# Kernel optimization log

Measured on AMD Instinct MI355X. Metric: run time of the kernel, lower is better.

The kernel has to match this reference:

```python
import jax, jax.numpy as jnp
import numpy as np

B = 4096      # batch (must equal hidden for the denom broadcast, see notes)
D = 2048      # input_size
P = 4096      # input_size * proj_factor
H = 4096      # hidden_size
NH = 16       # num_heads
HS = H // NH  # head_size = 256
EPS = 1e-5


def setup_inputs() -> dict:
    key = jax.random.key(0)
    ks = jax.random.split(key, 20)
    r = lambda i, shape, s=1.0: jax.random.normal(ks[i], shape, dtype=jnp.float32) * s
    w = 0.02
    return dict(
        x=r(0, (B, D)), h_prev=r(1, (B, H)), c_prev=r(2, (B, H)),
        n_prev=r(3, (B, H)), m_prev=r(4, (B, H)),
        ln_g=jnp.ones((D,), jnp.float32), ln_b=jnp.zeros((D,), jnp.float32),
        W_upL=r(5, (D, P), w), b_upL=jnp.zeros((P,), jnp.float32),
        W_upR=r(6, (D, H), w), b_upR=jnp.zeros((H,), jnp.float32),
        conv_w=r(7, (1, 1, 4), 0.5), conv_b=jnp.zeros((1,), jnp.float32),
        W_skip=r(8, (P, H), w), b_skip=jnp.zeros((H,), jnp.float32),
        Wq_w=r(9, (NH, P // NH, HS), w), Wq_b=jnp.zeros((H,), jnp.float32),
        Wk_w=r(10, (NH, P // NH, HS), w), Wk_b=jnp.zeros((H,), jnp.float32),
        Wv_w=r(11, (NH, P // NH, HS), w), Wv_b=jnp.zeros((H,), jnp.float32),
        Wi_w=r(12, (P, H), w), Wi_b=jnp.zeros((H,), jnp.float32),
        Wf_w=r(13, (P, H), w), Wf_b=jnp.zeros((H,), jnp.float32),
        Wo_w=r(14, (P, H), w), Wo_b=jnp.zeros((H,), jnp.float32),
        gn_g=jnp.ones((H,), jnp.float32), gn_b=jnp.zeros((H,), jnp.float32),
        W_down=r(15, (H, D), w), b_down=jnp.zeros((D,), jnp.float32),
    )


def _block_diag(x, w, b):
    # x: [B, nh*block_in], w: [nh, block_in, block_out] -> [B, nh*block_out]
    nh = w.shape[0]
    xr = x.reshape(x.shape[0], nh, -1)
    return jnp.einsum('bni,nio->bno', xr, w).reshape(x.shape[0], -1) + b


def reference(x, h_prev, c_prev, n_prev, m_prev, ln_g, ln_b,
              W_upL, b_upL, W_upR, b_upR, conv_w, conv_b, W_skip, b_skip,
              Wq_w, Wq_b, Wk_w, Wk_b, Wv_w, Wv_b,
              Wi_w, Wi_b, Wf_w, Wf_b, Wo_w, Wo_b,
              gn_g, gn_b, W_down, b_down):
    # LayerNorm over input_size
    mu = x.mean(-1, keepdims=True)
    var = x.var(-1, keepdims=True)
    x_norm = (x - mu) / jnp.sqrt(var + EPS) * ln_g + ln_b

    x_left = x_norm @ W_upL + b_upL    # [B, P]
    x_right = x_norm @ W_upR + b_upR   # [B, H]

    # CausalConv1D(1,1,4): left-pad 3 == pad both sides by 3 then trim right 3
    xc = jax.lax.conv_general_dilated(
        x_left[:, None, :], conv_w, (1,), [(3, 0)],
        dimension_numbers=('NCH', 'OIH', 'NCH')) + conv_b[None, :, None]
    x_conv = jax.nn.silu(xc[:, 0, :])  # [B, P]

    x_skip = x_conv @ W_skip + b_skip  # [B, H]

    q = _block_diag(x_conv, Wq_w, Wq_b)
    k = _block_diag(x_conv, Wk_w, Wk_b) / jnp.sqrt(jnp.float32(HS))
    v = _block_diag(x_left, Wv_w, Wv_b)

    i_tilde = x_conv @ Wi_w + Wi_b
    f_tilde = x_conv @ Wf_w + Wf_b
    o = jax.nn.sigmoid(x_left @ Wo_w + Wo_b)

    # stabilized exponential gating
    m_t = jnp.maximum(f_tilde + m_prev, i_tilde)
    i_g = jnp.exp(i_tilde - m_t)
    f_g = jnp.exp(f_tilde + m_prev - m_t)

    c_t = f_g * c_prev + i_g * (v * k)
    n_t = f_g * n_prev + i_g * k

    denom = jnp.maximum(jnp.abs(n_t.T @ q), 1.0)  # [H, H]; B == H so elementwise below
    h_t = o * (c_t * q) / denom                    # [B, H]

    # GroupNorm(num_heads, hidden) on 2D input [B, H]
    hg = h_t.reshape(B, NH, HS)
    gmu = hg.mean(-1, keepdims=True)
    gvar = hg.var(-1, keepdims=True)
    gn = ((hg - gmu) / jnp.sqrt(gvar + EPS)).reshape(B, H) * gn_g + gn_b

    out = (gn + x_skip) * jax.nn.silu(x_right)
    out = out @ W_down + b_down
    return (out + x, h_t, c_t, n_t, m_t)
```

## Files before the change

kernel.cpp:

```cpp
#include <hip/hip_runtime.h>
#include <math.h>

constexpr int BB = 4096;
constexpr int DD = 2048;
constexpr int PP = 4096;
constexpr int HH = 4096;
constexpr int NH = 16;
constexpr int HS = 256;

using bf16 = __bf16;
typedef __attribute__((ext_vector_type(8))) __bf16 bf16x8;
typedef __attribute__((ext_vector_type(2))) __bf16 bf16x2;
typedef __attribute__((ext_vector_type(4))) float  floatx4;

__device__ __forceinline__ void gl_lds16(const bf16* g, bf16* l) {
    __builtin_amdgcn_global_load_lds(
        (__attribute__((address_space(1))) void*)g,
        (__attribute__((address_space(3))) void*)l,
        16, 0, 0);
}

__global__ void ln_kernel(const float* __restrict__ x, const float* __restrict__ g,
                          const float* __restrict__ b, bf16* __restrict__ xn) {
    int row = blockIdx.x;
    int tid = threadIdx.x;
    const float* xr = x + (long)row * DD;
    float v[8];
    float s1 = 0.f, s2 = 0.f;
#pragma unroll
    for (int i = 0; i < 8; ++i) {
        v[i] = xr[tid + 256 * i];
        s1 += v[i]; s2 += v[i] * v[i];
    }
    for (int off = 32; off > 0; off >>= 1) {
        s1 += __shfl_down(s1, off);
        s2 += __shfl_down(s2, off);
    }
    __shared__ float r1[4], r2[4];
    if ((tid & 63) == 0) { r1[tid >> 6] = s1; r2[tid >> 6] = s2; }
    __syncthreads();
    float t1 = r1[0] + r1[1] + r1[2] + r1[3];
    float t2 = r2[0] + r2[1] + r2[2] + r2[3];
    float mu  = t1 * (1.f / DD);
    float var = t2 * (1.f / DD) - mu * mu;
    float inv = rsqrtf(var + 1e-5f);
    bf16* xo = xn + (long)row * DD;
#pragma unroll
    for (int i = 0; i < 8; ++i) {
        int c = tid + 256 * i;
        xo[c] = (bf16)((v[i] - mu) * inv * g[c] + b[c]);
    }
}

__global__ __launch_bounds__(256)
void tconv_kernel(const float* __restrict__ in, bf16* __restrict__ out, int R, int C) {
    __shared__ float t[64][33];
    const long zo = (long)blockIdx.z * (long)R * C;
    in  += zo; out += zo;
    const int c0 = blockIdx.x * 32, r0 = blockIdx.y * 64;
    const int xx = threadIdx.x & 31, yy = threadIdx.x >> 5;
#pragma unroll
    for (int d = 0; d < 64; d += 8)
        t[yy + d][xx] = in[(long)(r0 + yy + d) * C + c0 + xx];
    __syncthreads();
#pragma unroll
    for (int d = 0; d < 32; d += 8) {
        const int cc = c0 + yy + d;
        bf16x2 pk;
        pk.x = (bf16)t[2 * xx + 0][yy + d];
        pk.y = (bf16)t[2 * xx + 1][yy + d];
        *reinterpret_cast<bf16x2*>(&out[(long)cc * R + r0 + 2 * xx]) = pk;
    }
}

__global__ void conv_silu_kernel(const float* __restrict__ xl, const float* __restrict__ w,
                                 const float* __restrict__ cb, bf16* __restrict__ xc) {
    long i = (long)blockIdx.x * 256 + threadIdx.x;
    int p = (int)(i & (PP - 1));
    const float* base = xl + (i - p);
    float acc = cb[0];
#pragma unroll
    for (int j = 0; j < 4; ++j) {
        int pp = p - 3 + j;
        if (pp >= 0) acc = fmaf(w[j], base[pp], acc);
    }
    xc[i] = (bf16)(acc / (1.f + expf(-acc)));
}

__global__ void gates_kernel(const float* __restrict__ it_, const float* __restrict__ ft_,
                             const float* __restrict__ mp, const float* __restrict__ cp,
                             const float* __restrict__ np, const float* __restrict__ kk,
                             const float* __restrict__ vv,
                             float* __restrict__ c_out, float* __restrict__ n_out,
                             float* __restrict__ m_out) {
    long i = (long)blockIdx.x * 256 + threadIdx.x;
    float it = it_[i], ft = ft_[i];
    float fm = ft + mp[i];
    float mt = fmaxf(fm, it);
    float ig = expf(it - mt);
    float fg = expf(fm - mt);
    float ks = kk[i] * 0.0625f;
    c_out[i] = fg * cp[i] + ig * (vv[i] * ks);
    n_out[i] = fg * np[i] + ig * ks;
    m_out[i] = mt;
}

__global__ void hgn_kernel(const float* __restrict__ o_pre, const float* __restrict__ ct,
                           const float* __restrict__ qm, const float* __restrict__ den,
                           const float* __restrict__ xs, const float* __restrict__ xr,
                           const float* __restrict__ gg, const float* __restrict__ gb,
                           float* __restrict__ h_out, bf16* __restrict__ s_out) {
    int blk = blockIdx.x;
    int b = blk >> 4, hd = blk & 15;
    int c = threadIdx.x;
    int gcol = hd * HS + c;
    long idx = (long)b * HH + gcol;
    float o  = 1.f / (1.f + expf(-o_pre[idx]));
    float ht = o * ct[idx] * qm[idx] / fmaxf(fabsf(den[idx]), 1.f);
    h_out[idx] = ht;
    float s1 = ht, s2 = ht * ht;
    for (int off = 32; off > 0; off >>= 1) {
        s1 += __shfl_down(s1, off);
        s2 += __shfl_down(s2, off);
    }
    __shared__ float r1[4], r2[4];
    if ((c & 63) == 0) { r1[c >> 6] = s1; r2[c >> 6] = s2; }
    __syncthreads();
    float t1 = r1[0] + r1[1] + r1[2] + r1[3];
    float t2 = r2[0] + r2[1] + r2[2] + r2[3];
    float mu  = t1 * (1.f / HS);
    float var = t2 * (1.f / HS) - mu * mu;
    float gn  = (ht - mu) * rsqrtf(var + 1e-5f) * gg[gcol] + gb[gcol];
    float xrv = xr[idx];
    float sil = xrv / (1.f + expf(-xrv));
    s_out[idx] = (bf16)((gn + xs[idx]) * sil);
}

template<bool WRITE_BF16, bool ADD_RES>
__global__ __launch_bounds__(256)
void gemm_nt(const bf16* __restrict__ A, int lda, long sAz,
             const bf16* __restrict__ Bt, int ldb, long sBz,
             const float* __restrict__ bias, int sbz,
             const float* __restrict__ res,
             float* __restrict__ C, int ldc, long sCz,
             bf16* __restrict__ Cb, int ldcb, long sCbz,
             int K) {
    __shared__ bf16 As[128 * 32];
    __shared__ bf16 Bs[128 * 32];
    const int tid = threadIdx.x;
    const int m0 = blockIdx.y * 128, n0 = blockIdx.x * 128, z = blockIdx.z;
    A  += (long)z * sAz;
    Bt += (long)z * sBz;
    C  += (long)z * sCz;
    if (bias) bias += (long)z * sbz;
    if (WRITE_BF16) Cb += (long)z * sCbz;

    const int lane = tid & 63, wave = tid >> 6;
    const int row = tid >> 2;
    const int kc  = (tid & 3) * 8;
    const bf16* ga = A  + (long)(m0 + row) * lda + kc;
    const bf16* gb = Bt + (long)(n0 + row) * ldb + kc;
    bf16* lA = As + wave * (16 * 32);
    bf16* lB = Bs + wave * (16 * 32);
    const long stepA = (long)64 * lda, stepB = (long)64 * ldb;

    const int wm = (wave >> 1) * 64, wn = (wave & 1) * 64;
    const int lr = lane & 15, qd = lane >> 4;
    floatx4 acc[4][4] = {};

    for (int k0 = 0; k0 < K; k0 += 32) {
        gl_lds16(ga,         lA);
        gl_lds16(ga + stepA, lA + 64 * 32);
        gl_lds16(gb,         lB);
        gl_lds16(gb + stepB, lB + 64 * 32);
        ga += 32; gb += 32;
        __syncthreads();

        bf16x8 af[4], bfv[4];
#pragma unroll
        for (int i = 0; i < 4; ++i)
            af[i]  = *reinterpret_cast<const bf16x8*>(&As[(wm + i * 16 + lr) * 32 + qd * 8]);
#pragma unroll
        for (int j = 0; j < 4; ++j)
            bfv[j] = *reinterpret_cast<const bf16x8*>(&Bs[(wn + j * 16 + lr) * 32 + qd * 8]);
#pragma unroll
        for (int i = 0; i < 4; ++i)
#pragma unroll
            for (int j = 0; j < 4; ++j)
                acc[i][j] = __builtin_amdgcn_mfma_f32_16x16x32_bf16(af[i], bfv[j], acc[i][j], 0, 0, 0);
        __syncthreads();
    }

#pragma unroll
    for (int i = 0; i < 4; ++i) {
        const int rowb = m0 + wm + i * 16 + qd * 4;
#pragma unroll
        for (int j = 0; j < 4; ++j) {
            const int col = n0 + wn + j * 16 + lr;
            const float bi = bias ? bias[col] : 0.f;
#pragma unroll
            for (int r = 0; r < 4; ++r) {
                const long gi = (long)(rowb + r) * ldc + col;
                float v0 = acc[i][j][r] + bi;
                if (ADD_RES) v0 += res[gi];
                C[gi] = v0;
                if (WRITE_BF16) Cb[(long)(rowb + r) * ldcb + col] = (bf16)v0;
            }
        }
    }
}

extern "C" void kernel_launch(void* const* d_in, const int* in_sizes, int n_in,
                              void* d_out, int out_size, void* d_ws, size_t ws_size,
                              hipStream_t stream) {
    const float* x      = (const float*)d_in[0];
    const float* c_prev = (const float*)d_in[2];
    const float* n_prev = (const float*)d_in[3];
    const float* m_prev = (const float*)d_in[4];
    const float* ln_g   = (const float*)d_in[5];
    const float* ln_b   = (const float*)d_in[6];
    const float* W_upL  = (const float*)d_in[7];
    const float* b_upL  = (const float*)d_in[8];
    const float* W_upR  = (const float*)d_in[9];
    const float* b_upR  = (const float*)d_in[10];
    const float* conv_w = (const float*)d_in[11];
    const float* conv_b = (const float*)d_in[12];
    const float* W_skip = (const float*)d_in[13];
    const float* b_skip = (const float*)d_in[14];
    const float* Wq_w   = (const float*)d_in[15];
    const float* Wq_b   = (const float*)d_in[16];
    const float* Wk_w   = (const float*)d_in[17];
    const float* Wk_b   = (const float*)d_in[18];
    const float* Wv_w   = (const float*)d_in[19];
    const float* Wv_b   = (const float*)d_in[20];
    const float* Wi_w   = (const float*)d_in[21];
    const float* Wi_b   = (const float*)d_in[22];
    const float* Wf_w   = (const float*)d_in[23];
    const float* Wf_b   = (const float*)d_in[24];
    const float* Wo_w   = (const float*)d_in[25];
    const float* Wo_b   = (const float*)d_in[26];
    const float* gn_g   = (const float*)d_in[27];
    const float* gn_b   = (const float*)d_in[28];
    const float* W_down = (const float*)d_in[29];
    const float* b_down = (const float*)d_in[30];

    float* out0  = (float*)d_out;
    float* h_out = out0  + (long)BB * DD;
    float* c_out = h_out + (long)BB * HH;
    float* n_out = c_out + (long)BB * HH;
    float* m_out = n_out + (long)BB * HH;

    float* ws = (float*)d_ws;
    const long SLOT = (long)BB * HH;
    float* s0 = ws + 0 * SLOT;
    float* s1 = ws + 1 * SLOT;
    float* s2 = ws + 2 * SLOT;
    float* s3 = ws + 3 * SLOT;
    float* s4 = ws + 4 * SLOT;
    float* s5 = ws + 5 * SLOT;
    float* s6 = ws + 6 * SLOT;
    float* s7 = ws + 7 * SLOT;
    float* s8 = ws + 8 * SLOT;

    float* xr   = s0;
    float* xs   = s1;
    float* it   = s2;
    float* den  = s2;
    float* ft   = s3;
    float* opre = s4;
    float* qbuf = s5;
    float* kbuf = s6;
    float* xl   = s7;
    float* vbuf = s7;

    bf16* xn_bf = (bf16*)s6;
    bf16* xl_bf = (bf16*)(s6 + SLOT / 4);
    bf16* nT_bf = (bf16*)s3;
    bf16* qT_bf = (bf16*)(s3 + SLOT / 2);
    bf16* wt    = (bf16*)s8;
    bf16* xc_bf = (bf16*)(s8 + SLOT / 2);
    bf16* s_bf  = (bf16*)s7;

    dim3 blk(256);

    ln_kernel<<<BB, blk, 0, stream>>>(x, ln_g, ln_b, xn_bf);

    tconv_kernel<<<dim3(PP / 32, DD / 64, 1), blk, 0, stream>>>(W_upL, wt, DD, PP);
    gemm_nt<true, false><<<dim3(PP / 128, BB / 128, 1), blk, 0, stream>>>(
        xn_bf, DD, 0, wt, DD, 0, b_upL, 0, nullptr, xl, PP, 0, xl_bf, PP, 0, DD);

    tconv_kernel<<<dim3(HH / 32, DD / 64, 1), blk, 0, stream>>>(W_upR, wt, DD, HH);
    gemm_nt<false, false><<<dim3(HH / 128, BB / 128, 1), blk, 0, stream>>>(
        xn_bf, DD, 0, wt, DD, 0, b_upR, 0, nullptr, xr, HH, 0, nullptr, 0, 0, DD);

    conv_silu_kernel<<<dim3((unsigned)((long)BB * PP / 256)), blk, 0, stream>>>(
        xl, conv_w, conv_b, xc_bf);

    tconv_kernel<<<dim3(HH / 32, PP / 64, 1), blk, 0, stream>>>(W_skip, wt, PP, HH);
    gemm_nt<false, false><<<dim3(HH / 128, BB / 128, 1), blk, 0, stream>>>(
        xc_bf, PP, 0, wt, PP, 0, b_skip, 0, nullptr, xs, HH, 0, nullptr, 0, 0, PP);

    tconv_kernel<<<dim3(HH / 32, PP / 64, 1), blk, 0, stream>>>(Wi_w, wt, PP, HH);
    gemm_nt<false, false><<<dim3(HH / 128, BB / 128, 1), blk, 0, stream>>>(
        xc_bf, PP, 0, wt, PP, 0, Wi_b, 0, nullptr, it, HH, 0, nullptr, 0, 0, PP);

    tconv_kernel<<<dim3(HH / 32, PP / 64, 1), blk, 0, stream>>>(Wf_w, wt, PP, HH);
    gemm_nt<false, false><<<dim3(HH / 128, BB / 128, 1), blk, 0, stream>>>(
        xc_bf, PP, 0, wt, PP, 0, Wf_b, 0, nullptr, ft, HH, 0, nullptr, 0, 0, PP);

    tconv_kernel<<<dim3(HH / 32, PP / 64, 1), blk, 0, stream>>>(Wo_w, wt, PP, HH);
    gemm_nt<false, false><<<dim3(HH / 128, BB / 128, 1), blk, 0, stream>>>(
        xl_bf, PP, 0, wt, PP, 0, Wo_b, 0, nullptr, opre, HH, 0, nullptr, 0, 0, PP);

    tconv_kernel<<<dim3(HS / 32, HS / 64, NH), blk, 0, stream>>>(Wq_w, wt, HS, HS);
    gemm_nt<false, false><<<dim3(HS / 128, BB / 128, NH), blk, 0, stream>>>(
        xc_bf, PP, HS, wt, HS, (long)HS * HS, Wq_b, HS, nullptr, qbuf, HH, HS,
        nullptr, 0, 0, HS);

    tconv_kernel<<<dim3(HS / 32, HS / 64, NH), blk, 0, stream>>>(Wv_w, wt, HS, HS);
    gemm_nt<false, false><<<dim3(HS / 128, BB / 128, NH), blk, 0, stream>>>(
        xl_bf, PP, HS, wt, HS, (long)HS * HS, Wv_b, HS, nullptr, vbuf, HH, HS,
        nullptr, 0, 0, HS);

    tconv_kernel<<<dim3(HS / 32, HS / 64, NH), blk, 0, stream>>>(Wk_w, wt, HS, HS);
    gemm_nt<false, false><<<dim3(HS / 128, BB / 128, NH), blk, 0, stream>>>(
        xc_bf, PP, HS, wt, HS, (long)HS * HS, Wk_b, HS, nullptr, kbuf, HH, HS,
        nullptr, 0, 0, HS);

    gates_kernel<<<dim3((unsigned)((long)BB * HH / 256)), blk, 0, stream>>>(
        it, ft, m_prev, c_prev, n_prev, kbuf, vbuf, c_out, n_out, m_out);

    tconv_kernel<<<dim3(HH / 32, BB / 64, 1), blk, 0, stream>>>(n_out, nT_bf, BB, HH);
    tconv_kernel<<<dim3(HH / 32, BB / 64, 1), blk, 0, stream>>>(qbuf, qT_bf, BB, HH);

    gemm_nt<false, false><<<dim3(HH / 128, HH / 128, 1), blk, 0, stream>>>(
        nT_bf, BB, 0, qT_bf, BB, 0, nullptr, 0, nullptr, den, HH, 0,
        nullptr, 0, 0, BB);

    hgn_kernel<<<dim3(BB * NH), blk, 0, stream>>>(
        opre, c_out, qbuf, den, xs, xr, gn_g, gn_b, h_out, s_bf);

    tconv_kernel<<<dim3(DD / 32, HH / 64, 1), blk, 0, stream>>>(W_down, wt, HH, DD);
    gemm_nt<false, true><<<dim3(DD / 128, BB / 128, 1), blk, 0, stream>>>(
        s_bf, HH, 0, wt, HH, 0, b_down, 0, x, out0, DD, 0, nullptr, 0, 0, HH);
}
```

Baseline: 2.517 ms.

## Replace GEMM with 256x256 double-buffered pipelined MFMA kernel with swizzled LDS

Replaces the 128x128 single-buffered GEMM with a 512-thread 256x256 tile kernel. It uses K=64 stages split in two halves, double-buffered LDS filled by async global-to-LDS loads, and an XOR swizzle on the LDS layout to avoid bank conflicts. Loads for the next stage are issued between MFMA groups under s_setprio, with explicit vmcnt waits and barriers in place of __syncthreads. The aim is to hide memory latency, raise arithmetic intensity per tile, and improve L2 reuse through block remapping on 16x16 grids. The costs are heavy LDS use (128KB), more register pressure, and fewer blocks for the small per-head GEMMs.

```diff
diff --git a/kernel.cpp b/kernel.cpp
--- a/kernel.cpp
+++ b/kernel.cpp
@@ -19,6 +19,9 @@
         (__attribute__((address_space(3))) void*)l,
         16, 0, 0);
 }
+
+#define WAITV(n) asm volatile("s_waitcnt vmcnt(" #n ")" ::: "memory")
+#define BAR()    asm volatile("s_barrier" ::: "memory")
 
 __global__ void ln_kernel(const float* __restrict__ x, const float* __restrict__ g,
                           const float* __restrict__ b, bf16* __restrict__ xn) {
@@ -137,66 +140,132 @@
 }
 
 template<bool WRITE_BF16, bool ADD_RES>
-__global__ __launch_bounds__(256)
-void gemm_nt(const bf16* __restrict__ A, int lda, long sAz,
+__global__ __launch_bounds__(512, 2)
+void gemm256(const bf16* __restrict__ A, int lda, long sAz,
              const bf16* __restrict__ Bt, int ldb, long sBz,
              const float* __restrict__ bias, int sbz,
              const float* __restrict__ res,
              float* __restrict__ C, int ldc, long sCz,
              bf16* __restrict__ Cb, int ldcb, long sCbz,
              int K) {
-    __shared__ bf16 As[128 * 32];
-    __shared__ bf16 Bs[128 * 32];
-    const int tid = threadIdx.x;
-    const int m0 = blockIdx.y * 128, n0 = blockIdx.x * 128, z = blockIdx.z;
+    __shared__ bf16 smA[2][2][8192];
+    __shared__ bf16 smB[2][2][8192];
+
+    const int tid  = threadIdx.x;
+    const int wave = tid >> 6, lane = tid & 63;
+
+    int bx = blockIdx.x, by = blockIdx.y;
+    if (gridDim.x == 16 && gridDim.y == 16) {
+        int bid = by * 16 + bx;
+        int r = bid & 7, i = bid >> 3;
+        by = (r >> 1) * 4 + (i >> 3);
+        bx = (r & 1) * 8 + (i & 7);
+    }
+    const int m0 = by * 256, n0 = bx * 256, z = blockIdx.z;
     A  += (long)z * sAz;
     Bt += (long)z * sBz;
     C  += (long)z * sCz;
     if (bias) bias += (long)z * sbz;
     if (WRITE_BF16) Cb += (long)z * sCbz;
 
-    const int lane = tid & 63, wave = tid >> 6;
-    const int row = tid >> 2;
-    const int kc  = (tid & 3) * 8;
-    const bf16* ga = A  + (long)(m0 + row) * lda + kc;
-    const bf16* gb = Bt + (long)(n0 + row) * ldb + kc;
-    bf16* lA = As + wave * (16 * 32);
-    bf16* lB = Bs + wave * (16 * 32);
-    const long stepA = (long)64 * lda, stepB = (long)64 * ldb;
-
-    const int wm = (wave >> 1) * 64, wn = (wave & 1) * 64;
+    const int srow = tid >> 2;
+    const int scol = ((tid & 3) ^ ((tid >> 3) & 3)) * 8;
+    const bf16* pA = A  + (long)(m0 + srow) * lda + scol;
+    const bf16* pB = Bt + (long)(n0 + srow) * ldb + scol;
+
+#define STAGE_A(dd, kkk, kcol) do { \
+    const bf16* _s = pA + (kcol) + (kkk) * 32; \
+    gl_lds16(_s,                   &smA[dd][kkk][wave * 512]); \
+    gl_lds16(_s + 128 * (long)lda, &smA[dd][kkk][4096 + wave * 512]); } while (0)
+#define STAGE_B(dd, kkk, kcol) do { \
+    const bf16* _s = pB + (kcol) + (kkk) * 32; \
+    gl_lds16(_s,                   &smB[dd][kkk][wave * 512]); \
+    gl_lds16(_s + 128 * (long)ldb, &smB[dd][kkk][4096 + wave * 512]); } while (0)
+#define LD8(base, off) (*reinterpret_cast<const bf16x8*>((const char*)(base) + (off)))
+
+    const int wr = wave >> 2, wc = wave & 3;
     const int lr = lane & 15, qd = lane >> 4;
-    floatx4 acc[4][4] = {};
-
-    for (int k0 = 0; k0 < K; k0 += 32) {
-        gl_lds16(ga,         lA);
-        gl_lds16(ga + stepA, lA + 64 * 32);
-        gl_lds16(gb,         lB);
-        gl_lds16(gb + stepB, lB + 64 * 32);
-        ga += 32; gb += 32;
-        __syncthreads();
-
-        bf16x8 af[4], bfv[4];
+    const int xorv = ((lr >> 1) & 3) << 4;
+    const int aoff = (wr * 128 + lr) * 64 + ((qd * 16) ^ xorv);
+    const int boff = (wc * 64  + lr) * 64 + ((qd * 16) ^ xorv);
+
+    floatx4 acc[8][4] = {};
+    const int nt = K >> 6;
+
+    STAGE_A(0, 0, 0); STAGE_B(0, 0, 0); STAGE_A(0, 1, 0); STAGE_B(0, 1, 0);
+    WAITV(4);
+    BAR();
+
+    for (int t = 0; t < nt; ++t) {
+        const int d = t & 1, e = d ^ 1;
+        const int kn = (t + 1 < nt) ? (t + 1) * 64 : 0;
+        const char* A0p = (const char*)&smA[d][0][0];
+        const char* A1p = (const char*)&smA[d][1][0];
+        const char* B0p = (const char*)&smB[d][0][0];
+        const char* B1p = (const char*)&smB[d][1][0];
+        bf16x8 af[4], bv[4];
+
+#pragma unroll
+        for (int i = 0; i < 4; ++i) af[i] = LD8(A0p, aoff + i * 1024);
+#pragma unroll
+        for (int j = 0; j < 4; ++j) bv[j] = LD8(B0p, boff + j * 1024);
+        STAGE_A(e, 0, kn);
+        __builtin_amdgcn_s_setprio(1);
 #pragma unroll
         for (int i = 0; i < 4; ++i)
-            af[i]  = *reinterpret_cast<const bf16x8*>(&As[(wm + i * 16 + lr) * 32 + qd * 8]);
-#pragma unroll
-        for (int j = 0; j < 4; ++j)
-            bfv[j] = *reinterpret_cast<const bf16x8*>(&Bs[(wn + j * 16 + lr) * 32 + qd * 8]);
+#pragma unroll
+            for (int j = 0; j < 4; ++j)
+                acc[i][j] = __builtin_amdgcn_mfma_f32_16x16x32_bf16(af[i], bv[j], acc[i][j], 0, 0, 0);
+        __builtin_amdgcn_s_setprio(0);
+        BAR();
+
+#pragma unroll
+        for (int i = 0; i < 4; ++i) af[i] = LD8(A0p, aoff + 4096 + i * 1024);
+        STAGE_B(e, 0, kn);
+        __builtin_amdgcn_s_setprio(1);
 #pragma unroll
         for (int i = 0; i < 4; ++i)
 #pragma unroll
             for (int j = 0; j < 4; ++j)
-                acc[i][j] = __builtin_amdgcn_mfma_f32_16x16x32_bf16(af[i], bfv[j], acc[i][j], 0, 0, 0);
-        __syncthreads();
-    }
-
-#pragma unroll
-    for (int i = 0; i < 4; ++i) {
-        const int rowb = m0 + wm + i * 16 + qd * 4;
+                acc[4 + i][j] = __builtin_amdgcn_mfma_f32_16x16x32_bf16(af[i], bv[j], acc[4 + i][j], 0, 0, 0);
+        __builtin_amdgcn_s_setprio(0);
+        WAITV(4);
+        BAR();
+
+#pragma unroll
+        for (int i = 0; i < 4; ++i) af[i] = LD8(A1p, aoff + i * 1024);
+#pragma unroll
+        for (int j = 0; j < 4; ++j) bv[j] = LD8(B1p, boff + j * 1024);
+        STAGE_A(e, 1, kn);
+        __builtin_amdgcn_s_setprio(1);
+#pragma unroll
+        for (int i = 0; i < 4; ++i)
+#pragma unroll
+            for (int j = 0; j < 4; ++j)
+                acc[i][j] = __builtin_amdgcn_mfma_f32_16x16x32_bf16(af[i], bv[j], acc[i][j], 0, 0, 0);
+        __builtin_amdgcn_s_setprio(0);
+        BAR();
+
+#pragma unroll
+        for (int i = 0; i < 4; ++i) af[i] = LD8(A1p, aoff + 4096 + i * 1024);
+        STAGE_B(e, 1, kn);
+        __builtin_amdgcn_s_setprio(1);
+#pragma unroll
+        for (int i = 0; i < 4; ++i)
+#pragma unroll
+            for (int j = 0; j < 4; ++j)
+                acc[4 + i][j] = __builtin_amdgcn_mfma_f32_16x16x32_bf16(af[i], bv[j], acc[4 + i][j], 0, 0, 0);
+        __builtin_amdgcn_s_setprio(0);
+        WAITV(4);
+        BAR();
+    }
+
+#pragma unroll
+    for (int i = 0; i < 8; ++i) {
+        const int rowb = m0 + wr * 128 + i * 16 + qd * 4;
 #pragma unroll
         for (int j = 0; j < 4; ++j) {
-            const int col = n0 + wn + j * 16 + lr;
+            const int col = n0 + wc * 64 + j * 16 + lr;
             const float bi = bias ? bias[col] : 0.f;
 #pragma unroll
             for (int r = 0; r < 4; ++r) {
@@ -208,6 +277,9 @@
             }
         }
     }
+#undef STAGE_A
+#undef STAGE_B
+#undef LD8
 }
 
 extern "C" void kernel_launch(void* const* d_in, const int* in_sizes, int n_in,
@@ -282,48 +354,49 @@
     bf16* s_bf  = (bf16*)s7;
 
     dim3 blk(256);
+    dim3 gblk(512);
 
     ln_kernel<<<BB, blk, 0, stream>>>(x, ln_g, ln_b, xn_bf);
 
     tconv_kernel<<<dim3(PP / 32, DD / 64, 1), blk, 0, stream>>>(W_upL, wt, DD, PP);
-    gemm_nt<true, false><<<dim3(PP / 128, BB / 128, 1), blk, 0, stream>>>(
+    gemm256<true, false><<<dim3(PP / 256, BB / 256, 1), gblk, 0, stream>>>(
         xn_bf, DD, 0, wt, DD, 0, b_upL, 0, nullptr, xl, PP, 0, xl_bf, PP, 0, DD);
 
     tconv_kernel<<<dim3(HH / 32, DD / 64, 1), blk, 0, stream>>>(W_upR, wt, DD, HH);
-    gemm_nt<false, false><<<dim3(HH / 128, BB / 128, 1), blk, 0, stream>>>(
+    gemm256<false, false><<<dim3(HH / 256, BB / 256, 1), gblk, 0, stream>>>(
         xn_bf, DD, 0, wt, DD, 0, b_upR, 0, nullptr, xr, HH, 0, nullptr, 0, 0, DD);
 
     conv_silu_kernel<<<dim3((unsigned)((long)BB * PP / 256)), blk, 0, stream>>>(
         xl, conv_w, conv_b, xc_bf);
 
     tconv_kernel<<<dim3(HH / 32, PP / 64, 1), blk, 0, stream>>>(W_skip, wt, PP, HH);
-    gemm_nt<false, false><<<dim3(HH / 128, BB / 128, 1), blk, 0, stream>>>(
+    gemm256<false, false><<<dim3(HH / 256, BB / 256, 1), gblk, 0, stream>>>(
         xc_bf, PP, 0, wt, PP, 0, b_skip, 0, nullptr, xs, HH, 0, nullptr, 0, 0, PP);
 
     tconv_kernel<<<dim3(HH / 32, PP / 64, 1), blk, 0, stream>>>(Wi_w, wt, PP, HH);
-    gemm_nt<false, false><<<dim3(HH / 128, BB / 128, 1), blk, 0, stream>>>(
+    gemm256<false, false><<<dim3(HH / 256, BB / 256, 1), gblk, 0, stream>>>(
         xc_bf, PP, 0, wt, PP, 0, Wi_b, 0, nullptr, it, HH, 0, nullptr, 0, 0, PP);
 
     tconv_kernel<<<dim3(HH / 32, PP / 64, 1), blk, 0, stream>>>(Wf_w, wt, PP, HH);
-    gemm_nt<false, false><<<dim3(HH / 128, BB / 128, 1), blk, 0, stream>>>(
+    gemm256<false, false><<<dim3(HH / 256, BB / 256, 1), gblk, 0, stream>>>(
         xc_bf, PP, 0, wt, PP, 0, Wf_b, 0, nullptr, ft, HH, 0, nullptr, 0, 0, PP);
 
     tconv_kernel<<<dim3(HH / 32, PP / 64, 1), blk, 0, stream>>>(Wo_w, wt, PP, HH);
-    gemm_nt<false, false><<<dim3(HH / 128, BB / 128, 1), blk, 0, stream>>>(
+    gemm256<false, false><<<dim3(HH / 256, BB / 256, 1), gblk, 0, stream>>>(
         xl_bf, PP, 0, wt, PP, 0, Wo_b, 0, nullptr, opre, HH, 0, nullptr, 0, 0, PP);
 
     tconv_kernel<<<dim3(HS / 32, HS / 64, NH), blk, 0, stream>>>(Wq_w, wt, HS, HS);
-    gemm_nt<false, false><<<dim3(HS / 128, BB / 128, NH), blk, 0, stream>>>(
+    gemm256<false, false><<<dim3(1, BB / 256, NH), gblk, 0, stream>>>(
         xc_bf, PP, HS, wt, HS, (long)HS * HS, Wq_b, HS, nullptr, qbuf, HH, HS,
         nullptr, 0, 0, HS);
 
     tconv_kernel<<<dim3(HS / 32, HS / 64, NH), blk, 0, stream>>>(Wv_w, wt, HS, HS);
-    gemm_nt<false, false><<<dim3(HS / 128, BB / 128, NH), blk, 0, stream>>>(
+    gemm256<false, false><<<dim3(1, BB / 256, NH), gblk, 0, stream>>>(
         xl_bf, PP, HS, wt, HS, (long)HS * HS, Wv_b, HS, nullptr, vbuf, HH, HS,
         nullptr, 0, 0, HS);
 
     tconv_kernel<<<dim3(HS / 32, HS / 64, NH), blk, 0, stream>>>(Wk_w, wt, HS, HS);
-    gemm_nt<false, false><<<dim3(HS / 128, BB / 128, NH), blk, 0, stream>>>(
+    gemm256<false, false><<<dim3(1, BB / 256, NH), gblk, 0, stream>>>(
         xc_bf, PP, HS, wt, HS, (long)HS * HS, Wk_b, HS, nullptr, kbuf, HH, HS,
         nullptr, 0, 0, HS);
 
@@ -333,7 +406,7 @@
     tconv_kernel<<<dim3(HH / 32, BB / 64, 1), blk, 0, stream>>>(n_out, nT_bf, BB, HH);
     tconv_kernel<<<dim3(HH / 32, BB / 64, 1), blk, 0, stream>>>(qbuf, qT_bf, BB, HH);
 
-    gemm_nt<false, false><<<dim3(HH / 128, HH / 128, 1), blk, 0, stream>>>(
+    gemm256<false, false><<<dim3(HH / 256, HH / 256, 1), gblk, 0, stream>>>(
         nT_bf, BB, 0, qT_bf, BB, 0, nullptr, 0, nullptr, den, HH, 0,
         nullptr, 0, 0, BB);
 
@@ -341,6 +414,6 @@
         opre, c_out, qbuf, den, xs, xr, gn_g, gn_b, h_out, s_bf);
 
     tconv_kernel<<<dim3(DD / 32, HH / 64, 1), blk, 0, stream>>>(W_down, wt, HH, DD);
-    gemm_nt<false, true><<<dim3(DD / 128, BB / 128, 1), blk, 0, stream>>>(
+    gemm256<false, true><<<dim3(DD / 256, BB / 256, 1), gblk, 0, stream>>>(
         s_bf, HH, 0, wt, HH, 0, b_down, 0, x, out0, DD, 0, nullptr, 0, 0, HH);
 }
```

After: 2.017 ms. -19.9%, faster.
